# Performance work log

Measured on AMD Instinct MI355X. Metric: run time of the kernel, lower is better.

## Reference

```python
import jax, jax.numpy as jnp
import numpy as np
from jax import lax

HARD_RANK = 5
HARD_PROB = 0.5
MARGIN = 0.0
EPS = 1e-6  # F.pairwise_distance default eps (added to the difference)


def setup_inputs() -> dict:
    key = jax.random.key(0)
    x = jax.random.normal(key, (8192, 2, 256), dtype=jnp.float32)
    return {"x": x}


def _l2norm(v):
    # torch F.normalize: v / max(||v||, 1e-12)
    n = jnp.sqrt(jnp.sum(v * v, axis=1, keepdims=True))
    return v / jnp.maximum(n, 1e-12)


def reference(x):
    B, _, D = x.shape
    a = _l2norm(x[:, 0, :])  # anchors, unit norm -> ||a_i||^2 = 1
    p = _l2norm(x[:, 1, :])  # positives, unit norm

    # Full anchor-vs-positive distance matrix via GEMM (no [B,B,D] tensor).
    # torch pairwise_distance uses ||a - p + eps||, expand exactly:
    # ||a-p+eps*1||^2 = ||a||^2 + ||p||^2 - 2 a.p + 2*eps*(sum(a)-sum(p)) + D*eps^2
    am = lax.stop_gradient(a)
    pm = lax.stop_gradient(p)
    ip = am @ pm.T                          # [B, B]
    ra = jnp.sum(am, axis=1)                # [B]
    rp = jnp.sum(pm, axis=1)                # [B]
    d2 = 2.0 - 2.0 * ip + 2.0 * EPS * (ra[:, None] - rp[None, :]) + D * EPS * EPS
    dist = jnp.sqrt(jnp.maximum(d2, 0.0))

    # Exclude self (excidx drops idx) by masking diagonal to +inf.
    dmine = jnp.where(jnp.eye(B, dtype=bool), jnp.inf, dist)

    # hard_rank smallest distances per row (rank 0 = hardest negative).
    _, top_idx = lax.top_k(-dmine, HARD_RANK)   # [B, HARD_RANK]

    # With prob hard_prob pick the hardest; else uniform among top hard_rank.
    kr = jax.random.key(1)
    k1, k2 = jax.random.split(kr)
    coin = jax.random.uniform(k1, (B,)) < HARD_PROB
    rand_rank = jax.random.randint(k2, (B,), 0, HARD_RANK)
    rank = jnp.where(coin, 0, rand_rank)
    negidx = top_idx[jnp.arange(B), rank]       # [B]

    neg = p[negidx, :]
    pos_d2 = jnp.sum(jnp.square(a - p + EPS), axis=1)
    neg_d2 = jnp.sum(jnp.square(a - neg + EPS), axis=1)
    return jnp.mean(jax.nn.relu(pos_d2 - neg_d2 + MARGIN))
```

## Files before the change

kernel.cpp:

```cpp
#include <hip/hip_runtime.h>
#include <hip/hip_bf16.h>
#include <stdint.h>


#define NB 8192
#define NCG 32
#define EPSF 1e-6f
#define IMIN (-2147483647 - 1)

typedef int i32x4 __attribute__((ext_vector_type(4)));

struct U2 { uint32_t x, y; };

__host__ __device__ __forceinline__ uint32_t rotl32(uint32_t v, int n) {
  return (v << n) | (v >> (32 - n));
}

__host__ __device__ __forceinline__ U2 tf2x32(uint32_t k0, uint32_t k1,
                                              uint32_t x0, uint32_t x1) {
  uint32_t k2 = k0 ^ k1 ^ 0x1BD11BDAu;
#define TF_R(r) { x0 += x1; x1 = rotl32(x1, r); x1 ^= x0; }
  x0 += k0; x1 += k1;
  TF_R(13) TF_R(15) TF_R(26) TF_R(6)
  x0 += k1; x1 += k2 + 1u;
  TF_R(17) TF_R(29) TF_R(16) TF_R(24)
  x0 += k2; x1 += k0 + 2u;
  TF_R(13) TF_R(15) TF_R(26) TF_R(6)
  x0 += k0; x1 += k1 + 3u;
  TF_R(17) TF_R(29) TF_R(16) TF_R(24)
  x0 += k1; x1 += k2 + 4u;
  TF_R(13) TF_R(15) TF_R(26) TF_R(6)
  x0 += k2; x1 += k0 + 5u;
#undef TF_R
  U2 r; r.x = x0; r.y = x1; return r;
}

__device__ __forceinline__ uint32_t rng_word(U2 r) { return r.x ^ r.y; }

#define FINS5I(T0, T1, T2, T3, T4, C) {           \
    const int _c = (C), _t0 = T0, _t1 = T1, _t2 = T2, _t3 = T3, _t4 = T4; \
    T0 = _t0 > _c ? _t0 : _c;                     \
    asm("v_med3_i32 %0, %1, %2, %3" : "=v"(T1) : "v"(_c), "v"(_t0), "v"(_t1)); \
    asm("v_med3_i32 %0, %1, %2, %3" : "=v"(T2) : "v"(_c), "v"(_t1), "v"(_t2)); \
    asm("v_med3_i32 %0, %1, %2, %3" : "=v"(T3) : "v"(_c), "v"(_t2), "v"(_t3)); \
    asm("v_med3_i32 %0, %1, %2, %3" : "=v"(T4) : "v"(_c), "v"(_t3), "v"(_t4)); }

#define FINS5C(T0, T1, T2, T3, T4, C) {           \
    const int _t0 = T0, _t1 = T1, _t2 = T2, _t3 = T3, _t4 = T4, _c = C; \
    T0 = _t0 > _c ? _t0 : _c;                     \
    { const int m = _c < _t0 ? _c : _t0; T1 = _t1 > m ? _t1 : m; } \
    { const int m = _c < _t1 ? _c : _t1; T2 = _t2 > m ? _t2 : m; } \
    { const int m = _c < _t2 ? _c : _t2; T3 = _t3 > m ? _t3 : m; } \
    { const int m = _c < _t3 ? _c : _t3; T4 = _t4 > m ? _t4 : m; } }

__device__ __forceinline__ void gload16(const void* g, void* l) {
  __builtin_amdgcn_global_load_lds(
      (const __attribute__((address_space(1))) unsigned int*)g,
      (__attribute__((address_space(3))) unsigned int*)l, 16, 0, 0);
}

__global__ __launch_bounds__(256) void prep_kernel(
    const float* __restrict__ x,
    char* __restrict__ aq8, char* __restrict__ pq8) {
  const int w = threadIdx.x >> 6, l = threadIdx.x & 63;
  const int row = blockIdx.x * 4 + w;
  const float4* xr = (const float4*)(x + (size_t)row * 512);
  const float4 a4 = xr[l];
  const float4 p4 = xr[64 + l];
  float sa = a4.x * a4.x + a4.y * a4.y + a4.z * a4.z + a4.w * a4.w;
  float sp = p4.x * p4.x + p4.y * p4.y + p4.z * p4.z + p4.w * p4.w;
#pragma unroll
  for (int off = 32; off; off >>= 1) { sa += __shfl_xor(sa, off); sp += __shfl_xor(sp, off); }
  const float ia = 127.0f / fmaxf(sqrtf(sa), 1e-12f);
  const float ip_ = 127.0f / fmaxf(sqrtf(sp), 1e-12f);
  const int qa0 = (int)rintf(a4.x * ia), qa1 = (int)rintf(a4.y * ia);
  const int qa2 = (int)rintf(a4.z * ia), qa3 = (int)rintf(a4.w * ia);
  const int qp0 = (int)rintf(p4.x * ip_), qp1 = (int)rintf(p4.y * ip_);
  const int qp2 = (int)rintf(p4.z * ip_), qp3 = (int)rintf(p4.w * ip_);
  const uint32_t ua = (qa0 & 255) | ((qa1 & 255) << 8) |
                      ((qa2 & 255) << 16) | ((uint32_t)(qa3 & 255) << 24);
  const uint32_t up = (qp0 & 255) | ((qp1 & 255) << 8) |
                      ((qp2 & 255) << 16) | ((uint32_t)(qp3 & 255) << 24);
  *(uint32_t*)(aq8 + (size_t)row * 256 + l * 4) = ua;
  *(uint32_t*)(pq8 + (size_t)row * 256 + l * 4) = up;
}

__global__ __launch_bounds__(512, 2) void dist_topk_kernel(
    const char* __restrict__ aq8, const char* __restrict__ pq8,
    int* __restrict__ part) {
  __shared__ __align__(16) char smem[73728];

  const int tid = threadIdx.x;
  const int w = tid >> 6, l = tid & 63;
  const int lo = l & 15, hi = l >> 4;
  const int wr = w >> 2, wc = w & 3;

  const int b = blockIdx.x;
  const int xcd = b & 7, j = b >> 3;
  const int rb = (xcd >> 1) * 16 + (j >> 4);
  const int cb = (xcd & 1) * 16 + (j & 15);
  const int row0 = rb * 128, col0 = cb * 256;
  const bool hasDiag = (cb == (rb >> 1));

  i32x4 acc[4][4];
#pragma unroll
  for (int aq = 0; aq < 4; ++aq)
#pragma unroll
    for (int pq = 0; pq < 4; ++pq) { i32x4 z = {0, 0, 0, 0}; acc[aq][pq] = z; }

#define STAGE(BUF, KS)                                                        \
  {                                                                           \
    { const int off = tid * 16;                                               \
      const int R = off >> 7;                                                 \
      const int s = ((off >> 4) & 7) ^ (R & 7);                               \
      const int r = 2 * R + (s >> 2);                                         \
      const int kb = (s & 3) * 16;                                            \
      gload16(aq8 + (size_t)(row0 + r) * 256 + (KS) * 64 + kb,                \
              smem + (BUF) * 24576 + off); }                                  \
    _Pragma("unroll")                                                         \
    for (int jj = 0; jj < 2; ++jj) {                                          \
      const int off = jj * 8192 + tid * 16;                                   \
      const int R = off >> 7;                                                 \
      const int s = ((off >> 4) & 7) ^ (R & 7);                               \
      const int c = 2 * R + (s >> 2);                                         \
      const int kb = (s & 3) * 16;                                            \
      gload16(pq8 + (size_t)(col0 + c) * 256 + (KS) * 64 + kb,                \
              smem + (BUF) * 24576 + 8192 + off); }                           \
  }

#define LADDR(RR, T) (((RR) >> 1) * 128 + (((((RR) & 1) * 4 + (T)) ^ (((RR) >> 1) & 7)) * 16))

#define COMPUTE(BUF)                                                          \
  {                                                                           \
    i32x4 aF0, aF1, aF2, aF3, bF0, bF1, bF2, bF3;                             \
    { const int r = wr * 64 + 0 + lo;                                         \
      aF0 = __builtin_bit_cast(i32x4, *(const uint4*)(smem + (BUF) * 24576 + LADDR(r, hi))); } \
    { const int r = wr * 64 + 16 + lo;                                        \
      aF1 = __builtin_bit_cast(i32x4, *(const uint4*)(smem + (BUF) * 24576 + LADDR(r, hi))); } \
    { const int r = wr * 64 + 32 + lo;                                        \
      aF2 = __builtin_bit_cast(i32x4, *(const uint4*)(smem + (BUF) * 24576 + LADDR(r, hi))); } \
    { const int r = wr * 64 + 48 + lo;                                        \
      aF3 = __builtin_bit_cast(i32x4, *(const uint4*)(smem + (BUF) * 24576 + LADDR(r, hi))); } \
    { const int c = wc * 64 + 0 + lo;                                         \
      bF0 = __builtin_bit_cast(i32x4, *(const uint4*)(smem + (BUF) * 24576 + 8192 + LADDR(c, hi))); } \
    { const int c = wc * 64 + 16 + lo;                                        \
      bF1 = __builtin_bit_cast(i32x4, *(const uint4*)(smem + (BUF) * 24576 + 8192 + LADDR(c, hi))); } \
    __builtin_amdgcn_s_setprio(1);                                            \
    acc[0][0] = __builtin_amdgcn_mfma_i32_16x16x64_i8(bF0, aF0, acc[0][0], 0, 0, 0); \
    acc[1][0] = __builtin_amdgcn_mfma_i32_16x16x64_i8(bF0, aF1, acc[1][0], 0, 0, 0); \
    acc[2][0] = __builtin_amdgcn_mfma_i32_16x16x64_i8(bF0, aF2, acc[2][0], 0, 0, 0); \
    acc[3][0] = __builtin_amdgcn_mfma_i32_16x16x64_i8(bF0, aF3, acc[3][0], 0, 0, 0); \
    { const int c = wc * 64 + 32 + lo;                                        \
      bF2 = __builtin_bit_cast(i32x4, *(const uint4*)(smem + (BUF) * 24576 + 8192 + LADDR(c, hi))); } \
    acc[0][1] = __builtin_amdgcn_mfma_i32_16x16x64_i8(bF1, aF0, acc[0][1], 0, 0, 0); \
    acc[1][1] = __builtin_amdgcn_mfma_i32_16x16x64_i8(bF1, aF1, acc[1][1], 0, 0, 0); \
    acc[2][1] = __builtin_amdgcn_mfma_i32_16x16x64_i8(bF1, aF2, acc[2][1], 0, 0, 0); \
    acc[3][1] = __builtin_amdgcn_mfma_i32_16x16x64_i8(bF1, aF3, acc[3][1], 0, 0, 0); \
    { const int c = wc * 64 + 48 + lo;                                        \
      bF3 = __builtin_bit_cast(i32x4, *(const uint4*)(smem + (BUF) * 24576 + 8192 + LADDR(c, hi))); } \
    acc[0][2] = __builtin_amdgcn_mfma_i32_16x16x64_i8(bF2, aF0, acc[0][2], 0, 0, 0); \
    acc[1][2] = __builtin_amdgcn_mfma_i32_16x16x64_i8(bF2, aF1, acc[1][2], 0, 0, 0); \
    acc[2][2] = __builtin_amdgcn_mfma_i32_16x16x64_i8(bF2, aF2, acc[2][2], 0, 0, 0); \
    acc[3][2] = __builtin_amdgcn_mfma_i32_16x16x64_i8(bF2, aF3, acc[3][2], 0, 0, 0); \
    acc[0][3] = __builtin_amdgcn_mfma_i32_16x16x64_i8(bF3, aF0, acc[0][3], 0, 0, 0); \
    acc[1][3] = __builtin_amdgcn_mfma_i32_16x16x64_i8(bF3, aF1, acc[1][3], 0, 0, 0); \
    acc[2][3] = __builtin_amdgcn_mfma_i32_16x16x64_i8(bF3, aF2, acc[2][3], 0, 0, 0); \
    acc[3][3] = __builtin_amdgcn_mfma_i32_16x16x64_i8(bF3, aF3, acc[3][3], 0, 0, 0); \
    __builtin_amdgcn_s_setprio(0);                                            \
  }

#define WAITV3 { asm volatile("s_waitcnt vmcnt(3)" ::: "memory"); }
#define WAITV0 { asm volatile("s_waitcnt vmcnt(0)" ::: "memory"); }
#define BAR    { __builtin_amdgcn_s_barrier(); }

  STAGE(0, 0)
  STAGE(1, 1)
  WAITV3 BAR STAGE(2, 2) COMPUTE(0)
  WAITV3 BAR STAGE(0, 3) COMPUTE(1)
  WAITV3 BAR COMPUTE(2)
  WAITV0 BAR COMPUTE(0)

#undef STAGE
#undef LADDR
#undef COMPUTE
#undef WAITV3
#undef WAITV0
#undef BAR

  __syncthreads();
  int* mls = (int*)smem;
  const int vb13 = 8191 - (col0 + wc * 64) - hi * 4;

#define MINE_LOOP(DIAG)                                                       \
  _Pragma("unroll")                                                           \
  for (int aq = 0; aq < 4; ++aq) {                                            \
    int T0 = IMIN, T1 = IMIN, T2 = IMIN, T3 = IMIN, T4 = IMIN;                \
    const int arow = row0 + wr * 64 + aq * 16 + lo;                           \
    _Pragma("unroll")                                                         \
    for (int pq = 0; pq < 4; ++pq)                                            \
      _Pragma("unroll")                                                       \
      for (int rr = 0; rr < 4; ++rr) {                                        \
        int key = (int)(((uint32_t)acc[aq][pq][rr]) << 13) + vb13 - (pq * 16 + rr); \
        if (DIAG) {                                                           \
          if (col0 + wc * 64 + pq * 16 + hi * 4 + rr == arow) key = IMIN;     \
        }                                                                     \
        FINS5I(T0, T1, T2, T3, T4, key);                                      \
      }                                                                       \
    int* dst = mls + (wr * 64 + aq * 16 + lo) * 81 + (wc * 4 + hi) * 5;       \
    dst[0] = T0; dst[1] = T1; dst[2] = T2; dst[3] = T3; dst[4] = T4;          \
  }

  if (hasDiag) { MINE_LOOP(true) } else { MINE_LOOP(false) }
#undef MINE_LOOP
  __syncthreads();

  if (tid < 256) {
    const int row = tid >> 1, half = tid & 1;
    const int* s2 = mls + row * 81 + half * 40;
    int M0 = IMIN, M1 = IMIN, M2 = IMIN, M3 = IMIN, M4 = IMIN;
#pragma unroll
    for (int k = 0; k < 40; ++k) FINS5I(M0, M1, M2, M3, M4, s2[k]);
    const int c0 = __shfl_xor(M0, 1), c1 = __shfl_xor(M1, 1),
              c2 = __shfl_xor(M2, 1), c3 = __shfl_xor(M3, 1),
              c4 = __shfl_xor(M4, 1);
    FINS5I(M0, M1, M2, M3, M4, c0);
    FINS5I(M0, M1, M2, M3, M4, c1);
    FINS5I(M0, M1, M2, M3, M4, c2);
    FINS5I(M0, M1, M2, M3, M4, c3);
    FINS5I(M0, M1, M2, M3, M4, c4);
    if (half == 0) {
      int* dst = part + ((size_t)(row0 + row) * NCG + cb) * 5;
      dst[0] = M0; dst[1] = M1; dst[2] = M2; dst[3] = M3; dst[4] = M4;
    }
  }
}

__global__ __launch_bounds__(256) void merge_loss_kernel(
    const float* __restrict__ x, const int* __restrict__ part,
    float* __restrict__ rowloss,
    uint32_t k1a, uint32_t k1b, uint32_t k2a, uint32_t k2b) {
  const int w = threadIdx.x >> 6, l = threadIdx.x & 63;
  const int i = blockIdx.x * 4 + w;
  __shared__ int cs[4][160];
  const int* src = part + (size_t)i * (NCG * 5);
  cs[w][l] = src[l];
  cs[w][64 + l] = src[64 + l];
  if (l < 32) cs[w][128 + l] = src[128 + l];
  __syncthreads();

  int T0 = IMIN, T1 = IMIN, T2 = IMIN, T3 = IMIN, T4 = IMIN;
  for (int rch = 0; rch < NCG; ++rch) {
    for (int q = 0; q < 5; ++q) {
      const int c = cs[w][rch * 5 + q];
      if (c <= T4) break;
      FINS5C(T0, T1, T2, T3, T4, c);
    }
  }

  const uint32_t cw = rng_word(tf2x32(k1a, k1b, 0u, (uint32_t)i));
  const bool coin = (cw >> 31) == 0u;
  const uint32_t hb = rng_word(tf2x32(k2a, k2b, 0u, (uint32_t)i));
  const uint32_t lb = rng_word(tf2x32(k2a, k2b, 0u, (uint32_t)(NB + i)));
  const int rr = (int)(((hb % 5u) + (lb % 5u)) % 5u);
  const int rank = coin ? 0 : rr;
  const int kch = (rank == 0) ? T0 : (rank == 1) ? T1 : (rank == 2) ? T2
                : (rank == 3) ? T3 : T4;
  const int neg = 8191 - (kch & 8191);

  const float4 xa = *(const float4*)(x + (size_t)i * 512 + l * 4);
  const float4 xp = *(const float4*)(x + (size_t)i * 512 + 256 + l * 4);
  const float4 xn = *(const float4*)(x + (size_t)neg * 512 + 256 + l * 4);
  float sa = xa.x * xa.x + xa.y * xa.y + xa.z * xa.z + xa.w * xa.w;
  float sp = xp.x * xp.x + xp.y * xp.y + xp.z * xp.z + xp.w * xp.w;
  float sn = xn.x * xn.x + xn.y * xn.y + xn.z * xn.z + xn.w * xn.w;
#pragma unroll
  for (int off = 32; off; off >>= 1) {
    sa += __shfl_xor(sa, off); sp += __shfl_xor(sp, off); sn += __shfl_xor(sn, off);
  }
  const float na = fmaxf(sqrtf(sa), 1e-12f);
  const float np = fmaxf(sqrtf(sp), 1e-12f);
  const float nn = fmaxf(sqrtf(sn), 1e-12f);

  float pos = 0.f, ng = 0.f;
  {
    float av, pv, nv, dp, dn;
    av = xa.x / na; pv = xp.x / np; nv = xn.x / nn;
    dp = av - pv + EPSF; pos += dp * dp; dn = av - nv + EPSF; ng += dn * dn;
    av = xa.y / na; pv = xp.y / np; nv = xn.y / nn;
    dp = av - pv + EPSF; pos += dp * dp; dn = av - nv + EPSF; ng += dn * dn;
    av = xa.z / na; pv = xp.z / np; nv = xn.z / nn;
    dp = av - pv + EPSF; pos += dp * dp; dn = av - nv + EPSF; ng += dn * dn;
    av = xa.w / na; pv = xp.w / np; nv = xn.w / nn;
    dp = av - pv + EPSF; pos += dp * dp; dn = av - nv + EPSF; ng += dn * dn;
  }
#pragma unroll
  for (int off = 32; off; off >>= 1) {
    pos += __shfl_xor(pos, off); ng += __shfl_xor(ng, off);
  }
  if (l == 0) rowloss[i] = fmaxf(pos - ng, 0.0f);
}

__global__ __launch_bounds__(256) void finalize_kernel(
    const float* __restrict__ rowloss, float* __restrict__ out) {
  __shared__ float s[256];
  const int t = threadIdx.x;
  float a = 0.f;
  for (int k = 0; k < NB / 256; ++k) a += rowloss[t + 256 * k];
  s[t] = a;
  __syncthreads();
  for (int h = 128; h; h >>= 1) {
    if (t < h) s[t] += s[t + h];
    __syncthreads();
  }
  if (t == 0) out[0] = s[0] / (float)NB;
}

extern "C" void kernel_launch(void* const* d_in, const int* in_sizes, int n_in,
                              void* d_out, int out_size, void* d_ws, size_t ws_size,
                              hipStream_t stream) {
  (void)in_sizes; (void)n_in; (void)out_size; (void)ws_size;
  const float* x = (const float*)d_in[0];
  float* out = (float*)d_out;
  char* ws = (char*)d_ws;

  char* aq8 = ws;
  char* pq8 = ws + (size_t)2 * 1024 * 1024;
  int* part = (int*)(ws + (size_t)4 * 1024 * 1024);
  float* rowloss = (float*)(ws + (size_t)4 * 1024 * 1024 +
                            (size_t)NB * NCG * 5 * sizeof(int));

  U2 c0 = tf2x32(0u, 1u, 0u, 0u);
  U2 c1 = tf2x32(0u, 1u, 0u, 1u);
  const uint32_t k1a = c0.x, k1b = c0.y;
  const uint32_t k2a = c1.x, k2b = c1.y;

  prep_kernel<<<NB / 4, 256, 0, stream>>>(x, aq8, pq8);
  dist_topk_kernel<<<2048, 512, 0, stream>>>(aq8, pq8, part);
  merge_loss_kernel<<<NB / 4, 256, 0, stream>>>(x, part, rowloss, k1a, k1b, k2a, k2b);
  finalize_kernel<<<1, 256, 0, stream>>>(rowloss, out);
}
```

Measured before the change: 59.30 us.

## Load whole A tile upfront and give each wave a private B slice without barriers

The shared A panel for all four K-steps is now loaded once at the start, and each wave streams its own 64-column B slice into a private LDS region. Because each wave reuses only what it loaded itself, block-wide barriers between K-steps go away, leaving per-wave vmcnt/lgkmcnt waits. B tiles are now loaded redundantly by waves sharing a column group (wr=0/1), which doubles B global traffic, and each step has a single B buffer, so the next load overlaps only with MFMA issue. The LDS footprint shrinks from 72 KB to 64 KB.

```diff
diff --git a/kernel.cpp b/kernel.cpp
--- a/kernel.cpp
+++ b/kernel.cpp
@@ -88,7 +88,7 @@
 __global__ __launch_bounds__(512, 2) void dist_topk_kernel(
     const char* __restrict__ aq8, const char* __restrict__ pq8,
     int* __restrict__ part) {
-  __shared__ __align__(16) char smem[73728];
+  __shared__ __align__(16) char smem[65536];
 
   const int tid = threadIdx.x;
   const int w = tid >> 6, l = tid & 63;
@@ -102,62 +102,70 @@
   const int row0 = rb * 128, col0 = cb * 256;
   const bool hasDiag = (cb == (rb >> 1));
 
+  char* bReg = smem + 32768 + w * 4096;
+  const int bcol0 = col0 + wc * 64;
+
   i32x4 acc[4][4];
 #pragma unroll
   for (int aq = 0; aq < 4; ++aq)
 #pragma unroll
     for (int pq = 0; pq < 4; ++pq) { i32x4 z = {0, 0, 0, 0}; acc[aq][pq] = z; }
 
-#define STAGE(BUF, KS)                                                        \
+  {
+#pragma unroll
+    for (int jj = 0; jj < 4; ++jj) {
+      const int off = tid * 16;
+      const int R = off >> 7;
+      const int s = ((off >> 4) & 7) ^ (R & 7);
+      const int r = 2 * R + (s >> 2);
+      const int kb = (s & 3) * 16;
+      gload16(aq8 + (size_t)(row0 + r) * 256 + jj * 64 + kb,
+              smem + jj * 8192 + off);
+    }
+  }
+
+#define STAGE_B(KS)                                                           \
   {                                                                           \
-    { const int off = tid * 16;                                               \
-      const int R = off >> 7;                                                 \
-      const int s = ((off >> 4) & 7) ^ (R & 7);                               \
-      const int r = 2 * R + (s >> 2);                                         \
-      const int kb = (s & 3) * 16;                                            \
-      gload16(aq8 + (size_t)(row0 + r) * 256 + (KS) * 64 + kb,                \
-              smem + (BUF) * 24576 + off); }                                  \
     _Pragma("unroll")                                                         \
-    for (int jj = 0; jj < 2; ++jj) {                                          \
-      const int off = jj * 8192 + tid * 16;                                   \
+    for (int jj = 0; jj < 4; ++jj) {                                          \
+      const int off = jj * 1024 + l * 16;                                     \
       const int R = off >> 7;                                                 \
       const int s = ((off >> 4) & 7) ^ (R & 7);                               \
       const int c = 2 * R + (s >> 2);                                         \
       const int kb = (s & 3) * 16;                                            \
-      gload16(pq8 + (size_t)(col0 + c) * 256 + (KS) * 64 + kb,                \
-              smem + (BUF) * 24576 + 8192 + off); }                           \
+      gload16(pq8 + (size_t)(bcol0 + c) * 256 + (KS) * 64 + kb, bReg + off);  \
+    }                                                                         \
   }
 
 #define LADDR(RR, T) (((RR) >> 1) * 128 + (((((RR) & 1) * 4 + (T)) ^ (((RR) >> 1) & 7)) * 16))
 
-#define COMPUTE(BUF)                                                          \
+#define STEP(KS, STAGE_NEXT, NEXTKS)                                          \
   {                                                                           \
     i32x4 aF0, aF1, aF2, aF3, bF0, bF1, bF2, bF3;                             \
     { const int r = wr * 64 + 0 + lo;                                         \
-      aF0 = __builtin_bit_cast(i32x4, *(const uint4*)(smem + (BUF) * 24576 + LADDR(r, hi))); } \
+      aF0 = __builtin_bit_cast(i32x4, *(const uint4*)(smem + (KS) * 8192 + LADDR(r, hi))); } \
     { const int r = wr * 64 + 16 + lo;                                        \
-      aF1 = __builtin_bit_cast(i32x4, *(const uint4*)(smem + (BUF) * 24576 + LADDR(r, hi))); } \
+      aF1 = __builtin_bit_cast(i32x4, *(const uint4*)(smem + (KS) * 8192 + LADDR(r, hi))); } \
     { const int r = wr * 64 + 32 + lo;                                        \
-      aF2 = __builtin_bit_cast(i32x4, *(const uint4*)(smem + (BUF) * 24576 + LADDR(r, hi))); } \
+      aF2 = __builtin_bit_cast(i32x4, *(const uint4*)(smem + (KS) * 8192 + LADDR(r, hi))); } \
     { const int r = wr * 64 + 48 + lo;                                        \
-      aF3 = __builtin_bit_cast(i32x4, *(const uint4*)(smem + (BUF) * 24576 + LADDR(r, hi))); } \
-    { const int c = wc * 64 + 0 + lo;                                         \
-      bF0 = __builtin_bit_cast(i32x4, *(const uint4*)(smem + (BUF) * 24576 + 8192 + LADDR(c, hi))); } \
-    { const int c = wc * 64 + 16 + lo;                                        \
-      bF1 = __builtin_bit_cast(i32x4, *(const uint4*)(smem + (BUF) * 24576 + 8192 + LADDR(c, hi))); } \
+      aF3 = __builtin_bit_cast(i32x4, *(const uint4*)(smem + (KS) * 8192 + LADDR(r, hi))); } \
+    bF0 = __builtin_bit_cast(i32x4, *(const uint4*)(bReg + LADDR(0  + lo, hi))); \
+    bF1 = __builtin_bit_cast(i32x4, *(const uint4*)(bReg + LADDR(16 + lo, hi))); \
+    bF2 = __builtin_bit_cast(i32x4, *(const uint4*)(bReg + LADDR(32 + lo, hi))); \
+    bF3 = __builtin_bit_cast(i32x4, *(const uint4*)(bReg + LADDR(48 + lo, hi))); \
+    asm volatile("s_waitcnt lgkmcnt(0)" ::: "memory");                        \
+    __builtin_amdgcn_sched_barrier(0);                                        \
+    if (STAGE_NEXT) { STAGE_B(NEXTKS) }                                       \
     __builtin_amdgcn_s_setprio(1);                                            \
     acc[0][0] = __builtin_amdgcn_mfma_i32_16x16x64_i8(bF0, aF0, acc[0][0], 0, 0, 0); \
     acc[1][0] = __builtin_amdgcn_mfma_i32_16x16x64_i8(bF0, aF1, acc[1][0], 0, 0, 0); \
     acc[2][0] = __builtin_amdgcn_mfma_i32_16x16x64_i8(bF0, aF2, acc[2][0], 0, 0, 0); \
     acc[3][0] = __builtin_amdgcn_mfma_i32_16x16x64_i8(bF0, aF3, acc[3][0], 0, 0, 0); \
-    { const int c = wc * 64 + 32 + lo;                                        \
-      bF2 = __builtin_bit_cast(i32x4, *(const uint4*)(smem + (BUF) * 24576 + 8192 + LADDR(c, hi))); } \
     acc[0][1] = __builtin_amdgcn_mfma_i32_16x16x64_i8(bF1, aF0, acc[0][1], 0, 0, 0); \
     acc[1][1] = __builtin_amdgcn_mfma_i32_16x16x64_i8(bF1, aF1, acc[1][1], 0, 0, 0); \
     acc[2][1] = __builtin_amdgcn_mfma_i32_16x16x64_i8(bF1, aF2, acc[2][1], 0, 0, 0); \
     acc[3][1] = __builtin_amdgcn_mfma_i32_16x16x64_i8(bF1, aF3, acc[3][1], 0, 0, 0); \
-    { const int c = wc * 64 + 48 + lo;                                        \
-      bF3 = __builtin_bit_cast(i32x4, *(const uint4*)(smem + (BUF) * 24576 + 8192 + LADDR(c, hi))); } \
     acc[0][2] = __builtin_amdgcn_mfma_i32_16x16x64_i8(bF2, aF0, acc[0][2], 0, 0, 0); \
     acc[1][2] = __builtin_amdgcn_mfma_i32_16x16x64_i8(bF2, aF1, acc[1][2], 0, 0, 0); \
     acc[2][2] = __builtin_amdgcn_mfma_i32_16x16x64_i8(bF2, aF2, acc[2][2], 0, 0, 0); \
@@ -167,25 +175,21 @@
     acc[2][3] = __builtin_amdgcn_mfma_i32_16x16x64_i8(bF3, aF2, acc[2][3], 0, 0, 0); \
     acc[3][3] = __builtin_amdgcn_mfma_i32_16x16x64_i8(bF3, aF3, acc[3][3], 0, 0, 0); \
     __builtin_amdgcn_s_setprio(0);                                            \
-  }
-
-#define WAITV3 { asm volatile("s_waitcnt vmcnt(3)" ::: "memory"); }
-#define WAITV0 { asm volatile("s_waitcnt vmcnt(0)" ::: "memory"); }
-#define BAR    { __builtin_amdgcn_s_barrier(); }
-
-  STAGE(0, 0)
-  STAGE(1, 1)
-  WAITV3 BAR STAGE(2, 2) COMPUTE(0)
-  WAITV3 BAR STAGE(0, 3) COMPUTE(1)
-  WAITV3 BAR COMPUTE(2)
-  WAITV0 BAR COMPUTE(0)
-
-#undef STAGE
+    asm volatile("s_waitcnt vmcnt(0)" ::: "memory");                          \
+  }
+
+  STAGE_B(0)
+  asm volatile("s_waitcnt vmcnt(0)" ::: "memory");
+  __builtin_amdgcn_s_barrier();
+
+  STEP(0, 1, 1)
+  STEP(1, 1, 2)
+  STEP(2, 1, 3)
+  STEP(3, 0, 0)
+
+#undef STAGE_B
 #undef LADDR
-#undef COMPUTE
-#undef WAITV3
-#undef WAITV0
-#undef BAR
+#undef STEP
 
   __syncthreads();
   int* mls = (int*)smem;
```

Result: slower. 67.34 us (+13.6%).
